# Optimization experiments

Measured on AMD Instinct MI355X. Metric: run time of the kernel, lower is better.

The kernel has to match this reference:

```python
import jax, jax.numpy as jnp
import numpy as np


def setup_inputs() -> dict:
    key = jax.random.key(0)
    k1, k2, k3 = jax.random.split(key, 3)
    Na, Nb, D, K = 1024, 1024, 512, 256
    a = jax.random.normal(k1, (Na, D), dtype=jnp.float32)
    b = jax.random.normal(k2, (Nb, D), dtype=jnp.float32)
    feats = jax.random.normal(k3, (K, D), dtype=jnp.float32)
    return {"a": a, "b": b, "feats": feats}


def reference(a, b, feats):
    # 'ignorematch' mode of the Difference module.
    # Project both sets onto the feature bank: [Na,K] and [Nb,K]
    a_fk = jnp.matmul(a, feats.T)          # [Na, K]
    b_fk = jnp.matmul(b, feats.T)          # [Nb, K]
    a_e = a_fk[:, None, :]                 # [Na, 1, K]
    b_e = b_fk[None, :, :]                 # [1, Nb, K]
    # features present in a (>0) but absent in b (<=0)
    mask = ((a_e > 0) & (b_e <= 0)).astype(a_fk.dtype)  # [Na, Nb, K]
    result = jnp.sum(a_e * mask, axis=2)   # [Na, Nb]
    return result
```

## Files before the change

### kernel.cpp

```cpp
#include <hip/hip_runtime.h>
#include <hip/hip_bf16.h>


typedef short bf16x8 __attribute__((ext_vector_type(8)));
typedef float f32x4  __attribute__((ext_vector_type(4)));

#define BM 64
#define BN 64
#define BK 32
#define PAD 4

__global__ __launch_bounds__(256) void stage1_kernel(
    const float* __restrict__ a, const float* __restrict__ b,
    const float* __restrict__ feats, float* __restrict__ part)
{
    const int tile = blockIdx.x >> 2;
    const int ks   = blockIdx.x & 3;
    const int bm = tile >> 2;
    const int bn = tile & 3;
    const int m0 = bm * BM;
    const int n0 = bn * BN;

    const float* X = (m0 < 1024) ? (a + (size_t)m0 * 512)
                                 : (b + (size_t)(m0 - 1024) * 512);
    float* Out = part + (size_t)ks * 2048 * 256 + (size_t)m0 * 256;

    __shared__ float Xs[BK][BM + PAD];
    __shared__ float Fs[BK][BN + PAD];

    const int tid = threadIdx.x;
    const int tm = tid >> 4;
    const int tn = tid & 15;

    float acc[4][4];
    #pragma unroll
    for (int i = 0; i < 4; i++)
        #pragma unroll
        for (int j = 0; j < 4; j++) acc[i][j] = 0.f;

    const int kbase = ks * 128;
    for (int kt = 0; kt < 4; kt++) {
        const int k0 = kbase + kt * BK;
        #pragma unroll
        for (int r = 0; r < 2; r++) {
            int idx = tid + r * 256;
            int lm  = idx >> 3;
            int lk  = (idx & 7) * 4;
            float4 v = *(const float4*)(X + (size_t)lm * 512 + k0 + lk);
            Xs[lk + 0][lm] = v.x; Xs[lk + 1][lm] = v.y;
            Xs[lk + 2][lm] = v.z; Xs[lk + 3][lm] = v.w;
        }
        #pragma unroll
        for (int r = 0; r < 2; r++) {
            int idx = tid + r * 256;
            int ln  = idx >> 3;
            int lk  = (idx & 7) * 4;
            float4 v = *(const float4*)(feats + (size_t)(n0 + ln) * 512 + k0 + lk);
            Fs[lk + 0][ln] = v.x; Fs[lk + 1][ln] = v.y;
            Fs[lk + 2][ln] = v.z; Fs[lk + 3][ln] = v.w;
        }
        __syncthreads();

        #pragma unroll
        for (int kk = 0; kk < BK; kk++) {
            float xv[4], fv[4];
            #pragma unroll
            for (int i = 0; i < 4; i++) xv[i] = Xs[kk][tm * 4 + i];
            #pragma unroll
            for (int j = 0; j < 4; j++) fv[j] = Fs[kk][tn * 4 + j];
            #pragma unroll
            for (int i = 0; i < 4; i++)
                #pragma unroll
                for (int j = 0; j < 4; j++)
                    acc[i][j] += xv[i] * fv[j];
        }
        __syncthreads();
    }

    #pragma unroll
    for (int i = 0; i < 4; i++) {
        int row = tm * 4 + i;
        #pragma unroll
        for (int j = 0; j < 4; j++) {
            int col = n0 + tn * 4 + j;
            Out[row * 256 + col] = acc[i][j];
        }
    }
}

__global__ __launch_bounds__(256) void epilogue_kernel(
    const float* __restrict__ part,
    __hip_bfloat16* __restrict__ pbf, __hip_bfloat16* __restrict__ mbf)
{
    const int g = blockIdx.x * 256 + threadIdx.x;
    const int row = g >> 6;
    const int c4  = (g & 63) * 4;

    const float* base = part + (size_t)row * 256 + c4;
    float4 s = *(const float4*)base;
    #pragma unroll
    for (int sdx = 1; sdx < 4; sdx++) {
        float4 v = *(const float4*)(base + (size_t)sdx * 2048 * 256);
        s.x += v.x; s.y += v.y; s.z += v.z; s.w += v.w;
    }

    if (row < 1024) {
        __hip_bfloat16* o = pbf + (size_t)row * 256 + c4;
        o[0] = __float2bfloat16(fmaxf(s.x, 0.f));
        o[1] = __float2bfloat16(fmaxf(s.y, 0.f));
        o[2] = __float2bfloat16(fmaxf(s.z, 0.f));
        o[3] = __float2bfloat16(fmaxf(s.w, 0.f));
    } else {
        __hip_bfloat16* o = mbf + (size_t)(row - 1024) * 256 + c4;
        o[0] = __float2bfloat16(s.x <= 0.f ? 1.f : 0.f);
        o[1] = __float2bfloat16(s.y <= 0.f ? 1.f : 0.f);
        o[2] = __float2bfloat16(s.z <= 0.f ? 1.f : 0.f);
        o[3] = __float2bfloat16(s.w <= 0.f ? 1.f : 0.f);
    }
}

__global__ __launch_bounds__(256) void gemm2_kernel(
    const __hip_bfloat16* __restrict__ p, const __hip_bfloat16* __restrict__ m,
    float* __restrict__ out)
{
    const int bi = blockIdx.x >> 4;
    const int bj = blockIdx.x & 15;
    const int i0 = bi * 32;
    const int j0 = bj * 64;

    const int tid  = threadIdx.x;
    const int w    = tid >> 6;
    const int lane = tid & 63;
    const int wi = w >> 1;
    const int wj = w & 1;

    const int l15 = lane & 15;
    const int q   = lane >> 4;

    const int arow  = i0 + wi * 16 + l15;
    const int jbase = j0 + wj * 32;
    const int brow0 = jbase + l15;
    const int brow1 = brow0 + 16;

    const short* ps = (const short*)p;
    const short* ms = (const short*)m;

    f32x4 acc0 = {0.f, 0.f, 0.f, 0.f};
    f32x4 acc1 = {0.f, 0.f, 0.f, 0.f};

    #pragma unroll
    for (int k0 = 0; k0 < 256; k0 += 32) {
        const int ko = k0 + q * 8;
        bf16x8 av = *(const bf16x8*)(ps + (size_t)arow  * 256 + ko);
        bf16x8 b0 = *(const bf16x8*)(ms + (size_t)brow0 * 256 + ko);
        bf16x8 b1 = *(const bf16x8*)(ms + (size_t)brow1 * 256 + ko);
        acc0 = __builtin_amdgcn_mfma_f32_16x16x32_bf16(av, b0, acc0, 0, 0, 0);
        acc1 = __builtin_amdgcn_mfma_f32_16x16x32_bf16(av, b1, acc1, 0, 0, 0);
    }

    const int orow = i0 + wi * 16 + q * 4;
    const int ocol = jbase + l15;
    #pragma unroll
    for (int r = 0; r < 4; r++) {
        out[(size_t)(orow + r) * 1024 + ocol]      = acc0[r];
        out[(size_t)(orow + r) * 1024 + ocol + 16] = acc1[r];
    }
}

extern "C" void kernel_launch(void* const* d_in, const int* in_sizes, int n_in,
                              void* d_out, int out_size, void* d_ws, size_t ws_size,
                              hipStream_t stream) {
    const float* a     = (const float*)d_in[0];
    const float* b     = (const float*)d_in[1];
    const float* feats = (const float*)d_in[2];
    float* out = (float*)d_out;

    float* part = (float*)d_ws;
    __hip_bfloat16* pbf = (__hip_bfloat16*)((char*)d_ws + (size_t)8 * 1024 * 1024);
    __hip_bfloat16* mbf = pbf + 1024 * 256;

    stage1_kernel  <<<512, 256, 0, stream>>>(a, b, feats, part);
    epilogue_kernel<<<512, 256, 0, stream>>>(part, pbf, mbf);
    gemm2_kernel   <<<512, 256, 0, stream>>>(pbf, mbf, out);
}
```

Baseline: 81.42 us.

## Replace FP32 SIMT projection GEMM with split-bf16 MFMA emulation fused with epilogue

The FP32 SIMT first GEMM with split-K partials and a separate reduction epilogue is replaced. A conversion kernel now splits a, b and feats into bf16 hi/mid/lo parts, and an MFMA-based GEMM accumulates the cross products: three terms for the a side, six for the b side so the sign test stays accurate. ReLU and mask generation happen in that kernel's epilogue, which removes the FP32 partial buffer round trip and the separate reduction pass. The cost is extra conversion traffic and more MFMA work, plus a risk that sign decisions near zero differ from an exact FP32 result.

Result: slower. 88.34 us (+8.5%).

```diff
diff --git a/kernel.cpp b/kernel.cpp
--- a/kernel.cpp
+++ b/kernel.cpp
@@ -5,117 +5,129 @@
 typedef short bf16x8 __attribute__((ext_vector_type(8)));
 typedef float f32x4  __attribute__((ext_vector_type(4)));
 
-#define BM 64
-#define BN 64
-#define BK 32
-#define PAD 4
+__device__ inline void split3(float x, __hip_bfloat16& h, __hip_bfloat16& m, __hip_bfloat16& l) {
+    h = __float2bfloat16(x);
+    float r1 = x - __bfloat162float(h);
+    m = __float2bfloat16(r1);
+    float r2 = r1 - __bfloat162float(m);
+    l = __float2bfloat16(r2);
+}
+
+__global__ __launch_bounds__(256) void convert_kernel(
+    const float* __restrict__ a, const float* __restrict__ b, const float* __restrict__ f,
+    __hip_bfloat16* __restrict__ Ah, __hip_bfloat16* __restrict__ Am,
+    __hip_bfloat16* __restrict__ Bh, __hip_bfloat16* __restrict__ Bm, __hip_bfloat16* __restrict__ Bl,
+    __hip_bfloat16* __restrict__ Fh, __hip_bfloat16* __restrict__ Fm, __hip_bfloat16* __restrict__ Fl)
+{
+    const int t = blockIdx.x * 256 + threadIdx.x;
+    const int i4 = t * 4;
+
+    {
+        float4 v = *(const float4*)(a + i4);
+        __hip_bfloat16 h[4] __attribute__((aligned(8)));
+        __hip_bfloat16 m[4] __attribute__((aligned(8)));
+        __hip_bfloat16 l;
+        split3(v.x, h[0], m[0], l); split3(v.y, h[1], m[1], l);
+        split3(v.z, h[2], m[2], l); split3(v.w, h[3], m[3], l);
+        *(short4*)((short*)Ah + i4) = *(const short4*)h;
+        *(short4*)((short*)Am + i4) = *(const short4*)m;
+    }
+    {
+        float4 v = *(const float4*)(b + i4);
+        __hip_bfloat16 h[4] __attribute__((aligned(8)));
+        __hip_bfloat16 m[4] __attribute__((aligned(8)));
+        __hip_bfloat16 l[4] __attribute__((aligned(8)));
+        split3(v.x, h[0], m[0], l[0]); split3(v.y, h[1], m[1], l[1]);
+        split3(v.z, h[2], m[2], l[2]); split3(v.w, h[3], m[3], l[3]);
+        *(short4*)((short*)Bh + i4) = *(const short4*)h;
+        *(short4*)((short*)Bm + i4) = *(const short4*)m;
+        *(short4*)((short*)Bl + i4) = *(const short4*)l;
+    }
+    {
+        float x = f[t];
+        __hip_bfloat16 h, m, l;
+        split3(x, h, m, l);
+        Fh[t] = h; Fm[t] = m; Fl[t] = l;
+    }
+}
 
 __global__ __launch_bounds__(256) void stage1_kernel(
-    const float* __restrict__ a, const float* __restrict__ b,
-    const float* __restrict__ feats, float* __restrict__ part)
-{
-    const int tile = blockIdx.x >> 2;
-    const int ks   = blockIdx.x & 3;
-    const int bm = tile >> 2;
-    const int bn = tile & 3;
-    const int m0 = bm * BM;
-    const int n0 = bn * BN;
-
-    const float* X = (m0 < 1024) ? (a + (size_t)m0 * 512)
-                                 : (b + (size_t)(m0 - 1024) * 512);
-    float* Out = part + (size_t)ks * 2048 * 256 + (size_t)m0 * 256;
-
-    __shared__ float Xs[BK][BM + PAD];
-    __shared__ float Fs[BK][BN + PAD];
-
-    const int tid = threadIdx.x;
-    const int tm = tid >> 4;
-    const int tn = tid & 15;
-
-    float acc[4][4];
-    #pragma unroll
-    for (int i = 0; i < 4; i++)
-        #pragma unroll
-        for (int j = 0; j < 4; j++) acc[i][j] = 0.f;
-
-    const int kbase = ks * 128;
-    for (int kt = 0; kt < 4; kt++) {
-        const int k0 = kbase + kt * BK;
-        #pragma unroll
-        for (int r = 0; r < 2; r++) {
-            int idx = tid + r * 256;
-            int lm  = idx >> 3;
-            int lk  = (idx & 7) * 4;
-            float4 v = *(const float4*)(X + (size_t)lm * 512 + k0 + lk);
-            Xs[lk + 0][lm] = v.x; Xs[lk + 1][lm] = v.y;
-            Xs[lk + 2][lm] = v.z; Xs[lk + 3][lm] = v.w;
-        }
-        #pragma unroll
-        for (int r = 0; r < 2; r++) {
-            int idx = tid + r * 256;
-            int ln  = idx >> 3;
-            int lk  = (idx & 7) * 4;
-            float4 v = *(const float4*)(feats + (size_t)(n0 + ln) * 512 + k0 + lk);
-            Fs[lk + 0][ln] = v.x; Fs[lk + 1][ln] = v.y;
-            Fs[lk + 2][ln] = v.z; Fs[lk + 3][ln] = v.w;
-        }
-        __syncthreads();
-
-        #pragma unroll
-        for (int kk = 0; kk < BK; kk++) {
-            float xv[4], fv[4];
-            #pragma unroll
-            for (int i = 0; i < 4; i++) xv[i] = Xs[kk][tm * 4 + i];
-            #pragma unroll
-            for (int j = 0; j < 4; j++) fv[j] = Fs[kk][tn * 4 + j];
-            #pragma unroll
-            for (int i = 0; i < 4; i++)
-                #pragma unroll
-                for (int j = 0; j < 4; j++)
-                    acc[i][j] += xv[i] * fv[j];
-        }
-        __syncthreads();
-    }
-
-    #pragma unroll
-    for (int i = 0; i < 4; i++) {
-        int row = tm * 4 + i;
-        #pragma unroll
-        for (int j = 0; j < 4; j++) {
-            int col = n0 + tn * 4 + j;
-            Out[row * 256 + col] = acc[i][j];
-        }
-    }
-}
-
-__global__ __launch_bounds__(256) void epilogue_kernel(
-    const float* __restrict__ part,
+    const __hip_bfloat16* __restrict__ Ah, const __hip_bfloat16* __restrict__ Am,
+    const __hip_bfloat16* __restrict__ Bh, const __hip_bfloat16* __restrict__ Bm,
+    const __hip_bfloat16* __restrict__ Bl,
+    const __hip_bfloat16* __restrict__ Fh, const __hip_bfloat16* __restrict__ Fm,
+    const __hip_bfloat16* __restrict__ Fl,
     __hip_bfloat16* __restrict__ pbf, __hip_bfloat16* __restrict__ mbf)
 {
-    const int g = blockIdx.x * 256 + threadIdx.x;
-    const int row = g >> 6;
-    const int c4  = (g & 63) * 4;
-
-    const float* base = part + (size_t)row * 256 + c4;
-    float4 s = *(const float4*)base;
-    #pragma unroll
-    for (int sdx = 1; sdx < 4; sdx++) {
-        float4 v = *(const float4*)(base + (size_t)sdx * 2048 * 256);
-        s.x += v.x; s.y += v.y; s.z += v.z; s.w += v.w;
-    }
-
-    if (row < 1024) {
-        __hip_bfloat16* o = pbf + (size_t)row * 256 + c4;
-        o[0] = __float2bfloat16(fmaxf(s.x, 0.f));
-        o[1] = __float2bfloat16(fmaxf(s.y, 0.f));
-        o[2] = __float2bfloat16(fmaxf(s.z, 0.f));
-        o[3] = __float2bfloat16(fmaxf(s.w, 0.f));
+    const int idx = blockIdx.x;
+    const bool isA = idx < 256;
+    const int t  = idx & 255;
+    const int bi = t >> 3;
+    const int bn = t & 7;
+    const int m0 = bi * 32;
+    const int n0 = bn * 32;
+
+    const int tid  = threadIdx.x;
+    const int w    = tid >> 6;
+    const int lane = tid & 63;
+    const int wi = w >> 1, wj = w & 1;
+    const int l15 = lane & 15;
+    const int q   = lane >> 4;
+
+    const int ra = (m0 + wi * 16 + l15) * 512;
+    const int rf = (n0 + wj * 16 + l15) * 512;
+
+    f32x4 acc = {0.f, 0.f, 0.f, 0.f};
+
+    if (isA) {
+        const short* ah_p = (const short*)Ah + ra;
+        const short* am_p = (const short*)Am + ra;
+        const short* fh_p = (const short*)Fh + rf;
+        const short* fm_p = (const short*)Fm + rf;
+        #pragma unroll 4
+        for (int k0 = 0; k0 < 512; k0 += 32) {
+            const int ko = k0 + q * 8;
+            bf16x8 ah = *(const bf16x8*)(ah_p + ko);
+            bf16x8 am = *(const bf16x8*)(am_p + ko);
+            bf16x8 fh = *(const bf16x8*)(fh_p + ko);
+            bf16x8 fm = *(const bf16x8*)(fm_p + ko);
+            acc = __builtin_amdgcn_mfma_f32_16x16x32_bf16(ah, fh, acc, 0, 0, 0);
+            acc = __builtin_amdgcn_mfma_f32_16x16x32_bf16(ah, fm, acc, 0, 0, 0);
+            acc = __builtin_amdgcn_mfma_f32_16x16x32_bf16(am, fh, acc, 0, 0, 0);
+        }
+        const int orow = m0 + wi * 16 + q * 4;
+        const int ocol = n0 + wj * 16 + l15;
+        #pragma unroll
+        for (int r = 0; r < 4; r++)
+            pbf[(size_t)(orow + r) * 256 + ocol] = __float2bfloat16(fmaxf(acc[r], 0.f));
     } else {
-        __hip_bfloat16* o = mbf + (size_t)(row - 1024) * 256 + c4;
-        o[0] = __float2bfloat16(s.x <= 0.f ? 1.f : 0.f);
-        o[1] = __float2bfloat16(s.y <= 0.f ? 1.f : 0.f);
-        o[2] = __float2bfloat16(s.z <= 0.f ? 1.f : 0.f);
-        o[3] = __float2bfloat16(s.w <= 0.f ? 1.f : 0.f);
+        const short* bh_p = (const short*)Bh + ra;
+        const short* bm_p = (const short*)Bm + ra;
+        const short* bl_p = (const short*)Bl + ra;
+        const short* fh_p = (const short*)Fh + rf;
+        const short* fm_p = (const short*)Fm + rf;
+        const short* fl_p = (const short*)Fl + rf;
+        #pragma unroll 4
+        for (int k0 = 0; k0 < 512; k0 += 32) {
+            const int ko = k0 + q * 8;
+            bf16x8 bh = *(const bf16x8*)(bh_p + ko);
+            bf16x8 bm = *(const bf16x8*)(bm_p + ko);
+            bf16x8 bl = *(const bf16x8*)(bl_p + ko);
+            bf16x8 fh = *(const bf16x8*)(fh_p + ko);
+            bf16x8 fm = *(const bf16x8*)(fm_p + ko);
+            bf16x8 fl = *(const bf16x8*)(fl_p + ko);
+            acc = __builtin_amdgcn_mfma_f32_16x16x32_bf16(bh, fh, acc, 0, 0, 0);
+            acc = __builtin_amdgcn_mfma_f32_16x16x32_bf16(bh, fm, acc, 0, 0, 0);
+            acc = __builtin_amdgcn_mfma_f32_16x16x32_bf16(bm, fh, acc, 0, 0, 0);
+            acc = __builtin_amdgcn_mfma_f32_16x16x32_bf16(bh, fl, acc, 0, 0, 0);
+            acc = __builtin_amdgcn_mfma_f32_16x16x32_bf16(bl, fh, acc, 0, 0, 0);
+            acc = __builtin_amdgcn_mfma_f32_16x16x32_bf16(bm, fm, acc, 0, 0, 0);
+        }
+        const int orow = m0 + wi * 16 + q * 4;
+        const int ocol = n0 + wj * 16 + l15;
+        #pragma unroll
+        for (int r = 0; r < 4; r++)
+            mbf[(size_t)(orow + r) * 256 + ocol] = __float2bfloat16(acc[r] <= 0.f ? 1.f : 0.f);
     }
 }
 
@@ -131,9 +143,7 @@
     const int tid  = threadIdx.x;
     const int w    = tid >> 6;
     const int lane = tid & 63;
-    const int wi = w >> 1;
-    const int wj = w & 1;
-
+    const int wi = w >> 1, wj = w & 1;
     const int l15 = lane & 15;
     const int q   = lane >> 4;
 
@@ -175,11 +185,21 @@
     const float* feats = (const float*)d_in[2];
     float* out = (float*)d_out;
 
-    float* part = (float*)d_ws;
-    __hip_bfloat16* pbf = (__hip_bfloat16*)((char*)d_ws + (size_t)8 * 1024 * 1024);
+    const size_t NAB = 1024 * 512;
+    const size_t NF  = 256 * 512;
+    __hip_bfloat16* w0 = (__hip_bfloat16*)d_ws;
+    __hip_bfloat16* Ah = w0;
+    __hip_bfloat16* Am = Ah + NAB;
+    __hip_bfloat16* Bh = Am + NAB;
+    __hip_bfloat16* Bm = Bh + NAB;
+    __hip_bfloat16* Bl = Bm + NAB;
+    __hip_bfloat16* Fh = Bl + NAB;
+    __hip_bfloat16* Fm = Fh + NF;
+    __hip_bfloat16* Fl = Fm + NF;
+    __hip_bfloat16* pbf = Fl + NF;
     __hip_bfloat16* mbf = pbf + 1024 * 256;
 
-    stage1_kernel  <<<512, 256, 0, stream>>>(a, b, feats, part);
-    epilogue_kernel<<<512, 256, 0, stream>>>(part, pbf, mbf);
-    gemm2_kernel   <<<512, 256, 0, stream>>>(pbf, mbf, out);
-}
+    convert_kernel<<<512, 256, 0, stream>>>(a, b, feats, Ah, Am, Bh, Bm, Bl, Fh, Fm, Fl);
+    stage1_kernel <<<512, 256, 0, stream>>>(Ah, Am, Bh, Bm, Bl, Fh, Fm, Fl, pbf, mbf);
+    gemm2_kernel  <<<512, 256, 0, stream>>>(pbf, mbf, out);
+}
```
